# Performance work log

Hardware: AMD Instinct MI355X
Metric: run time of the kernel (lower is better)

The kernel has to match this reference:

```python
import jax, jax.numpy as jnp
import numpy as np

EPS = 1e-8
NUM_HEADS = 8
BELIEF_DIM = 256
TOP_K = 64
DEPTH_BIAS = 0.1


def setup_inputs() -> dict:
    key = jax.random.key(0)
    ks = jax.random.split(key, 12)
    B, T, H = 4, 2048, 2048
    N, D, h = 4096, BELIEF_DIM, NUM_HEADS
    G = 16
    s = 0.02
    return {
        'hidden': jax.random.normal(ks[0], (B, T, H), jnp.float32),
        'active_beliefs': jax.random.normal(ks[1], (N, D), jnp.float32),
        'goal_embeddings': jax.random.normal(ks[2], (G, D), jnp.float32),
        'goal_priorities': jax.random.uniform(ks[3], (G,), jnp.float32),
        'Wq': jax.random.normal(ks[4], (D * h, H), jnp.float32) * s,
        'Wo': jax.random.normal(ks[5], (H, D * h), jnp.float32) * s,
        'Wgoal': jax.random.normal(ks[6], (h, D), jnp.float32) * s,
        'log_temp': jnp.zeros((h,), jnp.float32),
        'Wu': jax.random.normal(ks[7], (H, D * h), jnp.float32) * s,
        'Wg1': jax.random.normal(ks[8], (H // 4, H), jnp.float32) * s,
        'bg1': jnp.zeros((H // 4,), jnp.float32),
        'Wg2': jax.random.normal(ks[9], (1, H // 4), jnp.float32) * s,
        'bg2': jnp.full((1,), 2.0, jnp.float32),  # read_gate_init_bias
        'conv_w': jax.random.normal(ks[10], (D * h, 1, 4), jnp.float32) * s,
    }


def reference(hidden, active_beliefs, goal_embeddings, goal_priorities,
              Wq, Wo, Wgoal, log_temp, Wu, Wg1, bg1, Wg2, bg2, conv_w):
    B, T, H = hidden.shape
    h, D = NUM_HEADS, BELIEF_DIM
    C = h * D

    # hyperspherical decomposition of active beliefs
    radii = jnp.maximum(jnp.linalg.norm(active_beliefs, axis=-1), EPS)  # [N]
    angles = active_beliefs / radii[:, None]                            # [N, D]

    # rough top-k selection (N_active > top_k path)
    mean_q = hidden.mean(axis=(0, 1)) @ Wq.T                 # [h*D]
    rough_q = mean_q.reshape(h, D).mean(axis=0)              # [D]
    rough_scores = angles @ rough_q                          # [N]
    _, topk = jax.lax.top_k(rough_scores, TOP_K)
    keys = angles[topk]              # [K, D]
    values = active_beliefs[topk]    # [K, D]

    # read gate: Linear -> ReLU -> Linear, then signed-sqrt + sigmoid
    g = jax.nn.relu(hidden @ Wg1.T + bg1) @ Wg2.T + bg2      # [B, T, 1]
    g = jnp.sign(g) * jnp.sqrt(jnp.maximum(jnp.abs(g), 1e-6))
    gate = jax.nn.sigmoid(g)

    # per-head queries and temperature-scaled Hopfield scores
    queries = (hidden @ Wq.T).reshape(B, T, h, D)
    temp = jnp.maximum(jnp.exp(log_temp + DEPTH_BIAS), 0.1)  # [h]
    scores = jnp.einsum('bthd,nd->bthn', queries, keys) / jnp.sqrt(jnp.float32(D))
    scores = scores * temp[None, None, :, None]

    # goal-directed bias
    goal_radii = jnp.maximum(jnp.linalg.norm(goal_embeddings, axis=-1), EPS)
    goal_angles = goal_embeddings / goal_radii[:, None]      # [G, D]
    sim = (keys @ goal_angles.T) * goal_priorities[None, :]  # [K, G]
    max_goal_sim = sim.max(axis=-1)                          # [K]
    gate_w = jax.nn.sigmoid(Wgoal @ goal_angles.mean(axis=0))  # [h]
    goal_bias = gate_w[:, None] * max_goal_sim[None, :]      # [h, K]
    scores = scores + goal_bias[None, None, :, :]

    attn = jax.nn.softmax(scores, axis=-1)                   # [B, T, h, K]
    retrieved = jnp.einsum('bthn,nd->bthd', attn, values)    # [B, T, h, D]
    flat = retrieved.reshape(B, T, C)

    # depthwise causal conv (kernel=4, left pad 3) + SiLU fusion
    x = jnp.transpose(flat, (0, 2, 1))                       # [B, C, T]
    conv = jax.lax.conv_general_dilated(
        x, conv_w, window_strides=(1,), padding=[(3, 0)],
        feature_group_count=C, dimension_numbers=('NCH', 'OIH', 'NCH'))
    flat = flat + jax.nn.silu(jnp.transpose(conv, (0, 2, 1)))

    output = gate * (flat @ Wo.T)                            # [B, T, H]
    utility_logits = flat @ Wu.T                             # [B, T, H]
    return output, utility_logits, attn, retrieved
```

## Files before the change

kernel.cpp:

```cpp
#include <hip/hip_runtime.h>


typedef unsigned short ushort_t;
typedef unsigned int   uint_t;

typedef __bf16 bf16x8 __attribute__((ext_vector_type(8)));
typedef float  f32x4  __attribute__((ext_vector_type(4)));
typedef unsigned short u16x8 __attribute__((ext_vector_type(8)));
typedef unsigned short u16x4 __attribute__((ext_vector_type(4)));

#define DI static __device__ __forceinline__

DI ushort_t f2bf(float f) {
    union { float f; uint_t u; } v; v.f = f;
    uint_t u = v.u;
    uint_t r = (u + 0x7FFFu + ((u >> 16) & 1u)) >> 16;
    return (ushort_t)r;
}
DI float bf2f(ushort_t b) {
    union { uint_t u; float f; } v; v.u = ((uint_t)b) << 16;
    return v.f;
}

#define GLL16(gp, lp) __builtin_amdgcn_global_load_lds( \
    (const __attribute__((address_space(1))) void*)(gp), \
    (__attribute__((address_space(3))) void*)(lp), 16, 0, 0)

constexpr int BT  = 8192;
constexpr int Hd  = 2048;
constexpr int Dd  = 256;
constexpr int Cd  = 2048;

constexpr size_t O_HID     = 0;
constexpr size_t O_WQ      = 33554432;
constexpr size_t O_WOWU    = 41943040;
constexpr size_t O_WG1     = 58720256;
constexpr size_t O_QRY     = 60817408;
constexpr size_t O_MEANACC = 94371840;
constexpr size_t O_MEANQ   = 94380032;
constexpr size_t O_RAD     = 94389248;
constexpr size_t O_RSC     = 94405632;
constexpr size_t O_KEYS    = 94422016;
constexpr size_t O_VALT    = 94454784;
constexpr size_t O_GB      = 94487552;
constexpr size_t O_HS      = 94489600;
constexpr size_t O_GP      = 94489856;

__global__ void cast4_kernel(const float* __restrict__ sA, ushort_t* __restrict__ dA, int nA,
                             const float* __restrict__ sB, ushort_t* __restrict__ dB, int nB,
                             const float* __restrict__ sC, ushort_t* __restrict__ dC, int nC,
                             const float* __restrict__ sD, ushort_t* __restrict__ dD, int nD) {
    int total = (nA + nB + nC + nD) >> 2;
    for (int i = blockIdx.x * blockDim.x + threadIdx.x; i < total;
         i += gridDim.x * blockDim.x) {
        int e = i * 4;
        const float* s; ushort_t* d;
        if (e < nA)              { s = sA + e; d = dA + e; }
        else if ((e -= nA) < nB) { s = sB + e; d = dB + e; }
        else if ((e -= nB) < nC) { s = sC + e; d = dC + e; }
        else                     { e -= nC; s = sD + e; d = dD + e; }
        float4 v = *(const float4*)s;
        u16x4 o;
        o[0] = f2bf(v.x); o[1] = f2bf(v.y); o[2] = f2bf(v.z); o[3] = f2bf(v.w);
        *(u16x4*)d = o;
    }
}

__global__ void cast_hidden_kernel(const float* __restrict__ hid, ushort_t* __restrict__ hbf,
                                   float* __restrict__ macc) {
    int r0 = blockIdx.x * 32;
    float s[8];
#pragma unroll
    for (int j = 0; j < 8; ++j) s[j] = 0.f;
    for (int r = 0; r < 32; ++r) {
        const float* rp = hid + (size_t)(r0 + r) * Hd;
        ushort_t*    wp = hbf + (size_t)(r0 + r) * Hd;
#pragma unroll
        for (int j = 0; j < 2; ++j) {
            int c = j * 1024 + threadIdx.x * 4;
            float4 v = *(const float4*)(rp + c);
            s[j*4+0] += v.x; s[j*4+1] += v.y; s[j*4+2] += v.z; s[j*4+3] += v.w;
            u16x4 o;
            o[0] = f2bf(v.x); o[1] = f2bf(v.y); o[2] = f2bf(v.z); o[3] = f2bf(v.w);
            *(u16x4*)(wp + c) = o;
        }
    }
#pragma unroll
    for (int j = 0; j < 2; ++j)
#pragma unroll
        for (int q = 0; q < 4; ++q)
            atomicAdd(macc + j * 1024 + threadIdx.x * 4 + q, s[j*4+q]);
}

__global__ void meanq_kernel(const float* __restrict__ macc, const float* __restrict__ Wq,
                             float* __restrict__ mq) {
    int wid = blockIdx.x * 4 + (threadIdx.x >> 6);
    int lane = threadIdx.x & 63;
    const float inv = 1.f / 8192.f;
    float s = 0.f;
    for (int k = lane; k < Hd; k += 64) s += macc[k] * inv * Wq[(size_t)wid * Hd + k];
#pragma unroll
    for (int m = 32; m; m >>= 1) s += __shfl_xor(s, m, 64);
    if (lane == 0) mq[wid] = s;
}

__global__ void beliefs_kernel(const float* __restrict__ ab, const float* __restrict__ mq,
                               float* __restrict__ radii, float* __restrict__ rsc) {
    int n = blockIdx.x * 4 + (threadIdx.x >> 6);
    int lane = threadIdx.x & 63;
    float rqv[4];
#pragma unroll
    for (int j = 0; j < 4; ++j) {
        int d = lane + 64 * j;
        float s = 0.f;
#pragma unroll
        for (int hh = 0; hh < 8; ++hh) s += mq[hh * 256 + d];
        rqv[j] = s * 0.125f;
    }
    float v[4]; float r2 = 0.f;
#pragma unroll
    for (int j = 0; j < 4; ++j) { v[j] = ab[(size_t)n * Dd + lane + 64 * j]; r2 += v[j] * v[j]; }
#pragma unroll
    for (int m = 32; m; m >>= 1) r2 += __shfl_xor(r2, m, 64);
    float r = fmaxf(sqrtf(r2), 1e-8f);
    float dq = 0.f;
#pragma unroll
    for (int j = 0; j < 4; ++j) dq += (v[j] / r) * rqv[j];
#pragma unroll
    for (int m = 32; m; m >>= 1) dq += __shfl_xor(dq, m, 64);
    if (lane == 0) { radii[n] = r; rsc[n] = dq; }
}

__global__ void topk_kernel(const float* __restrict__ ab, const float* __restrict__ radii,
                            const float* __restrict__ rsc, const float* __restrict__ gemb,
                            const float* __restrict__ gprio, const float* __restrict__ Wgoal,
                            const float* __restrict__ ltemp,
                            ushort_t* __restrict__ keysg, ushort_t* __restrict__ valtg,
                            float* __restrict__ gbias, float* __restrict__ hscale) {
    __shared__ float s_sc[4096];
    __shared__ float s_rv[4];
    __shared__ int   s_ri[4];
    __shared__ int   s_top[64];
    __shared__ float s_ga[16 * 256];
    __shared__ float s_mga[256];
    __shared__ float s_gw[8];
    __shared__ float s_keyf[64 * 256];
    __shared__ float s_red[256];

    int t = threadIdx.x;
    int lane = t & 63, w = t >> 6;
    for (int it = 0; it < 16; ++it) s_sc[t + it * 256] = rsc[t + it * 256];
    __syncthreads();

    for (int kk = 0; kk < 64; ++kk) {
        float bv = -3.4e38f; int bi = 0x7fffffff;
#pragma unroll
        for (int j = 0; j < 16; ++j) {
            int idx = t * 16 + j;
            float v = s_sc[idx];
            if (v > bv || (v == bv && idx < bi)) { bv = v; bi = idx; }
        }
#pragma unroll
        for (int m = 32; m; m >>= 1) {
            float ov = __shfl_xor(bv, m, 64);
            int   oi = __shfl_xor(bi, m, 64);
            if (ov > bv || (ov == bv && oi < bi)) { bv = ov; bi = oi; }
        }
        if (lane == 0) { s_rv[w] = bv; s_ri[w] = bi; }
        __syncthreads();
        if (t == 0) {
            float fv = s_rv[0]; int fi = s_ri[0];
#pragma unroll
            for (int wv = 1; wv < 4; ++wv)
                if (s_rv[wv] > fv || (s_rv[wv] == fv && s_ri[wv] < fi)) { fv = s_rv[wv]; fi = s_ri[wv]; }
            s_top[kk] = fi; s_sc[fi] = -3.4e38f;
        }
        __syncthreads();
    }

    {
        int kk = t >> 2, dp = t & 3;
        int idx = s_top[kk];
        float r = radii[idx];
        for (int dd = 0; dd < 64; ++dd) {
            int d = dp * 64 + dd;
            float v = ab[(size_t)idx * Dd + d];
            float kf = v / r;
            s_keyf[kk * 256 + d] = kf;
            keysg[kk * 256 + d] = f2bf(kf);
            valtg[d * 64 + kk]  = f2bf(v);
        }
    }
    {
        for (int g = w; g < 16; g += 4) {
            float v[4]; float r2 = 0.f;
#pragma unroll
            for (int j = 0; j < 4; ++j) { v[j] = gemb[g * 256 + lane + 64 * j]; r2 += v[j] * v[j]; }
#pragma unroll
            for (int m = 32; m; m >>= 1) r2 += __shfl_xor(r2, m, 64);
            float r = fmaxf(sqrtf(r2), 1e-8f);
#pragma unroll
            for (int j = 0; j < 4; ++j) s_ga[g * 256 + lane + 64 * j] = v[j] / r;
        }
    }
    __syncthreads();
    {
        float s = 0.f;
        for (int g = 0; g < 16; ++g) s += s_ga[g * 256 + t];
        s_mga[t] = s * (1.f / 16.f);
    }
    __syncthreads();
    if (t < 8) {
        float s = 0.f;
        for (int d = 0; d < 256; ++d) s += Wgoal[t * 256 + d] * s_mga[d];
        s_gw[t] = 1.f / (1.f + expf(-s));
        hscale[t] = fmaxf(expf(ltemp[t] + 0.1f), 0.1f) * (1.f / 16.f);
    }
    __syncthreads();
    {
        int kk = t & 63, gq = t >> 6;
        float best = -3.4e38f;
        for (int g = gq * 4; g < gq * 4 + 4; ++g) {
            float dot = 0.f;
            for (int d = 0; d < 256; ++d) dot += s_keyf[kk * 256 + d] * s_ga[g * 256 + d];
            best = fmaxf(best, dot * gprio[g]);
        }
        s_red[t] = best;
    }
    __syncthreads();
    if (t < 64) {
        float m = fmaxf(fmaxf(s_red[t], s_red[t + 64]), fmaxf(s_red[t + 128], s_red[t + 192]));
        for (int hh = 0; hh < 8; ++hh) gbias[hh * 64 + t] = s_gw[hh] * m;
    }
}

template <int EPI>
__global__ __launch_bounds__(256)
void gemm_bt_kernel(const ushort_t* __restrict__ A, const ushort_t* __restrict__ Bw,
                    const ushort_t* __restrict__ Bw2, int Kd,
                    ushort_t* __restrict__ obf, float* __restrict__ of1, float* __restrict__ of2,
                    const float* __restrict__ bg1, const float* __restrict__ Wg2,
                    float* __restrict__ gpart, const float* __restrict__ bg2) {
    __shared__ ushort_t lA[128 * 32];
    __shared__ ushort_t lB[128 * 32];
    const int tid = threadIdx.x;
    const int lane = tid & 63;
    const int w = tid >> 6;
    const int wr = (w >> 1) * 64, wc = (w & 1) * 64;

    const int nwg = gridDim.x * gridDim.y;
    const int lin = blockIdx.y * gridDim.x + blockIdx.x;
    const int swz = (lin & 7) * (nwg >> 3) + (lin >> 3);
    const int bm = (swz / gridDim.x) * 128, bn = (swz % gridDim.x) * 128;

    f32x4 acc[4][4];
#pragma unroll
    for (int mi = 0; mi < 4; ++mi)
#pragma unroll
        for (int ni = 0; ni < 4; ++ni)
#pragma unroll
            for (int q = 0; q < 4; ++q) acc[mi][ni][q] = 0.f;

    const ushort_t* Ab = A + (size_t)bm * Kd;
    const ushort_t* Bb;
    if (EPI == 3 && bn >= 2048) Bb = Bw2 + (size_t)(bn - 2048) * Kd;
    else                        Bb = Bw + (size_t)bn * Kd;
    const int c0 = tid, c1 = tid + 256;

    for (int kt = 0; kt < Kd; kt += 32) {
        __syncthreads();
        GLL16(Ab + (size_t)(c0 >> 2) * Kd + kt + (c0 & 3) * 8, lA + c0 * 8);
        GLL16(Ab + (size_t)(c1 >> 2) * Kd + kt + (c1 & 3) * 8, lA + c1 * 8);
        GLL16(Bb + (size_t)(c0 >> 2) * Kd + kt + (c0 & 3) * 8, lB + c0 * 8);
        GLL16(Bb + (size_t)(c1 >> 2) * Kd + kt + (c1 & 3) * 8, lB + c1 * 8);
        __syncthreads();
        const int ko = (lane >> 4) * 8;
        bf16x8 af[4], bf[4];
#pragma unroll
        for (int mi = 0; mi < 4; ++mi)
            af[mi] = *(const bf16x8*)&lA[(wr + mi * 16 + (lane & 15)) * 32 + ko];
#pragma unroll
        for (int ni = 0; ni < 4; ++ni)
            bf[ni] = *(const bf16x8*)&lB[(wc + ni * 16 + (lane & 15)) * 32 + ko];
#pragma unroll
        for (int mi = 0; mi < 4; ++mi)
#pragma unroll
            for (int ni = 0; ni < 4; ++ni)
                acc[mi][ni] = __builtin_amdgcn_mfma_f32_16x16x32_bf16(af[mi], bf[ni], acc[mi][ni], 0, 0, 0);
    }

    if (EPI == 2) {
        const float b2 = bg2[0];
#pragma unroll
        for (int mi = 0; mi < 4; ++mi)
#pragma unroll
            for (int r = 0; r < 4; ++r) {
                int row = bm + wr + mi * 16 + (lane >> 4) * 4 + r;
                float g = gpart[row] + b2;
                float sg = (g > 0.f) ? 1.f : ((g < 0.f) ? -1.f : 0.f);
                float ss = sg * sqrtf(fmaxf(fabsf(g), 1e-6f));
                float gv = 1.f / (1.f + expf(-ss));
#pragma unroll
                for (int ni = 0; ni < 4; ++ni) {
                    int col = bn + wc + ni * 16 + (lane & 15);
                    float v = acc[mi][ni][r];
                    if (col < 2048) of1[(size_t)row * 2048 + col] = gv * v;
                    else            of2[(size_t)row * 2048 + (col - 2048)] = v;
                }
            }
    } else {
        if (bn < 2048) {
#pragma unroll
            for (int mi = 0; mi < 4; ++mi)
#pragma unroll
                for (int ni = 0; ni < 4; ++ni)
#pragma unroll
                    for (int r = 0; r < 4; ++r) {
                        int row = bm + wr + mi * 16 + (lane >> 4) * 4 + r;
                        int col = bn + wc + ni * 16 + (lane & 15);
                        obf[(size_t)row * 2048 + col] = f2bf(acc[mi][ni][r]);
                    }
        } else {
            float wg[4], bb[4];
#pragma unroll
            for (int ni = 0; ni < 4; ++ni) {
                int col = bn + wc + ni * 16 + (lane & 15) - 2048;
                wg[ni] = Wg2[col]; bb[ni] = bg1[col];
            }
#pragma unroll
            for (int mi = 0; mi < 4; ++mi)
#pragma unroll
                for (int r = 0; r < 4; ++r) {
                    float s = 0.f;
#pragma unroll
                    for (int ni = 0; ni < 4; ++ni) {
                        float v = acc[mi][ni][r] + bb[ni];
                        v = fmaxf(v, 0.f);
                        s += v * wg[ni];
                    }
#pragma unroll
                    for (int m = 8; m; m >>= 1) s += __shfl_xor(s, m, 64);
                    if ((lane & 15) == 0)
                        atomicAdd(gpart + bm + wr + mi * 16 + (lane >> 4) * 4 + r, s);
                }
        }
    }
}

__global__ __launch_bounds__(256, 1)
void attn_kernel(const ushort_t* __restrict__ qry, const ushort_t* __restrict__ keysg,
                 const ushort_t* __restrict__ valtg, const float* __restrict__ gbias,
                 const float* __restrict__ hscale, float* __restrict__ attn_out,
                 float* __restrict__ retr_out, ushort_t* __restrict__ flatb) {
    __shared__ ushort_t sK[64 * 256];
    __shared__ ushort_t sV[256 * 64];
    __shared__ ushort_t sQ[4][32 * 256];
    __shared__ ushort_t sP[4][32 * 64];

    const int tid = threadIdx.x, lane = tid & 63, w = tid >> 6;
    const int r0 = blockIdx.x * 32;

    for (int it = 0; it < 8; ++it) {
        int f = it * 256 + tid;
        int row = f >> 5, cb = f & 31;
        u16x8 v = *(const u16x8*)(keysg + f * 8);
        int byte = (row * 512 + cb * 16) ^ ((row & 7) << 4);
        *(u16x8*)((char*)sK + byte) = v;
    }
    for (int it = 0; it < 8; ++it) {
        int f = it * 256 + tid;
        int row = f >> 3, cb = f & 7;
        u16x8 v = *(const u16x8*)(valtg + f * 8);
        int byte = (row * 128 + cb * 16) ^ ((row & 7) << 4);
        *(u16x8*)((char*)sV + byte) = v;
    }
    __syncthreads();

    char* sQw = (char*)sQ[w];
    char* sPw = (char*)sP[w];

    for (int hi = 0; hi < 2; ++hi) {
        const int head = w * 2 + hi;
        const float hs = hscale[head];
        float gb[4];
#pragma unroll
        for (int ni = 0; ni < 4; ++ni) gb[ni] = gbias[head * 64 + ni * 16 + (lane & 15)];

        for (int it = 0; it < 16; ++it) {
            int f = it * 64 + lane;
            int row = f >> 5, cb = f & 31;
            u16x8 v = *(const u16x8*)(qry + (size_t)(r0 + row) * Cd + head * 256 + cb * 8);
            int byte = (row * 512 + cb * 16) ^ ((row & 7) << 4);
            *(u16x8*)(sQw + byte) = v;
        }

        f32x4 accs[2][4];
#pragma unroll
        for (int mi = 0; mi < 2; ++mi)
#pragma unroll
            for (int ni = 0; ni < 4; ++ni)
#pragma unroll
                for (int q = 0; q < 4; ++q) accs[mi][ni][q] = 0.f;

        for (int kt = 0; kt < 8; ++kt) {
            const int kb = kt * 64 + (lane >> 4) * 16;
            bf16x8 aq[2], bk[4];
#pragma unroll
            for (int mi = 0; mi < 2; ++mi) {
                int m = mi * 16 + (lane & 15);
                aq[mi] = *(const bf16x8*)(sQw + ((m * 512 + kb) ^ ((m & 7) << 4)));
            }
#pragma unroll
            for (int ni = 0; ni < 4; ++ni) {
                int n = ni * 16 + (lane & 15);
                bk[ni] = *(const bf16x8*)((const char*)sK + ((n * 512 + kb) ^ ((n & 7) << 4)));
            }
#pragma unroll
            for (int mi = 0; mi < 2; ++mi)
#pragma unroll
                for (int ni = 0; ni < 4; ++ni)
                    accs[mi][ni] = __builtin_amdgcn_mfma_f32_16x16x32_bf16(aq[mi], bk[ni], accs[mi][ni], 0, 0, 0);
        }

#pragma unroll
        for (int mi = 0; mi < 2; ++mi)
#pragma unroll
            for (int r = 0; r < 4; ++r) {
                float sc[4];
                float mx = -3.4e38f;
#pragma unroll
                for (int ni = 0; ni < 4; ++ni) {
                    sc[ni] = accs[mi][ni][r] * hs + gb[ni];
                    mx = fmaxf(mx, sc[ni]);
                }
#pragma unroll
                for (int m = 8; m; m >>= 1) mx = fmaxf(mx, __shfl_xor(mx, m, 64));
                float p[4]; float sm = 0.f;
#pragma unroll
                for (int ni = 0; ni < 4; ++ni) { p[ni] = expf(sc[ni] - mx); sm += p[ni]; }
#pragma unroll
                for (int m = 8; m; m >>= 1) sm += __shfl_xor(sm, m, 64);
                float inv = 1.f / sm;
                int row = mi * 16 + (lane >> 4) * 4 + r;
                size_t ob = (size_t)(r0 + row) * 512 + head * 64;
#pragma unroll
                for (int ni = 0; ni < 4; ++ni) {
                    float a = p[ni] * inv;
                    int col = ni * 16 + (lane & 15);
                    attn_out[ob + col] = a;
                    int byte = (row * 128 + col * 2) ^ ((row & 7) << 4);
                    *(ushort_t*)(sPw + byte) = f2bf(a);
                }
            }

        f32x4 accr[2][16];
#pragma unroll
        for (int mi = 0; mi < 2; ++mi)
#pragma unroll
            for (int ni = 0; ni < 16; ++ni)
#pragma unroll
                for (int q = 0; q < 4; ++q) accr[mi][ni][q] = 0.f;

#pragma unroll
        for (int kt = 0; kt < 2; ++kt) {
            const int kb = kt * 64 + (lane >> 4) * 16;
            bf16x8 ap[2];
#pragma unroll
            for (int mi = 0; mi < 2; ++mi) {
                int m = mi * 16 + (lane & 15);
                ap[mi] = *(const bf16x8*)(sPw + ((m * 128 + kb) ^ ((m & 7) << 4)));
            }
#pragma unroll
            for (int ni = 0; ni < 16; ++ni) {
                int n = ni * 16 + (lane & 15);
                bf16x8 bv = *(const bf16x8*)((const char*)sV + ((n * 128 + kb) ^ ((n & 7) << 4)));
                accr[0][ni] = __builtin_amdgcn_mfma_f32_16x16x32_bf16(ap[0], bv, accr[0][ni], 0, 0, 0);
                accr[1][ni] = __builtin_amdgcn_mfma_f32_16x16x32_bf16(ap[1], bv, accr[1][ni], 0, 0, 0);
            }
        }

#pragma unroll
        for (int mi = 0; mi < 2; ++mi)
#pragma unroll
            for (int ni = 0; ni < 16; ++ni)
#pragma unroll
                for (int r = 0; r < 4; ++r) {
                    int row = mi * 16 + (lane >> 4) * 4 + r;
                    int d = ni * 16 + (lane & 15);
                    float v = accr[mi][ni][r];
                    size_t o = (size_t)(r0 + row) * Cd + head * 256 + d;
                    retr_out[o] = v;
                    flatb[o] = f2bf(v);
                }
    }
}

__global__ void conv_kernel(const ushort_t* __restrict__ flat, const float* __restrict__ cw,
                            ushort_t* __restrict__ flat2) {
    int cq = blockIdx.x * 256 + threadIdx.x;
    int c  = cq * 4;
    int b  = blockIdx.z;
    int t0 = blockIdx.y * 32;
    float4 wv[4];
#pragma unroll
    for (int j = 0; j < 4; ++j) wv[j] = *(const float4*)(cw + (size_t)(c + j) * 4);
    size_t base = (size_t)b * 2048 * Cd + c;
    float xm3[4], xm2[4], xm1[4];
    if (t0 == 0) {
#pragma unroll
        for (int j = 0; j < 4; ++j) { xm3[j] = 0.f; xm2[j] = 0.f; xm1[j] = 0.f; }
    } else {
        u16x4 a3 = *(const u16x4*)(flat + base + (size_t)(t0 - 3) * Cd);
        u16x4 a2 = *(const u16x4*)(flat + base + (size_t)(t0 - 2) * Cd);
        u16x4 a1 = *(const u16x4*)(flat + base + (size_t)(t0 - 1) * Cd);
#pragma unroll
        for (int j = 0; j < 4; ++j) { xm3[j] = bf2f(a3[j]); xm2[j] = bf2f(a2[j]); xm1[j] = bf2f(a1[j]); }
    }
    for (int t = t0; t < t0 + 32; ++t) {
        u16x4 xv = *(const u16x4*)(flat + base + (size_t)t * Cd);
        u16x4 ov;
#pragma unroll
        for (int j = 0; j < 4; ++j) {
            float x = bf2f(xv[j]);
            float cv = wv[j].x * xm3[j] + wv[j].y * xm2[j] + wv[j].z * xm1[j] + wv[j].w * x;
            float sl = cv / (1.f + expf(-cv));
            ov[j] = f2bf(x + sl);
            xm3[j] = xm2[j]; xm2[j] = xm1[j]; xm1[j] = x;
        }
        *(u16x4*)(flat2 + base + (size_t)t * Cd) = ov;
    }
}

extern "C" void kernel_launch(void* const* d_in, const int* in_sizes, int n_in,
                              void* d_out, int out_size, void* d_ws, size_t ws_size,
                              hipStream_t stream) {
    (void)in_sizes; (void)n_in; (void)out_size; (void)ws_size;
    const float* hid   = (const float*)d_in[0];
    const float* ab    = (const float*)d_in[1];
    const float* gemb  = (const float*)d_in[2];
    const float* gprio = (const float*)d_in[3];
    const float* Wq    = (const float*)d_in[4];
    const float* Wo    = (const float*)d_in[5];
    const float* Wgoal = (const float*)d_in[6];
    const float* ltemp = (const float*)d_in[7];
    const float* Wu    = (const float*)d_in[8];
    const float* Wg1   = (const float*)d_in[9];
    const float* bg1   = (const float*)d_in[10];
    const float* Wg2   = (const float*)d_in[11];
    const float* bg2   = (const float*)d_in[12];
    const float* cw    = (const float*)d_in[13];

    float* out      = (float*)d_out;
    float* out_util = out + 16777216;
    float* out_attn = out + 33554432;
    float* out_retr = out + 37748736;

    char* ws = (char*)d_ws;
    ushort_t* hbf    = (ushort_t*)(ws + O_HID);
    ushort_t* wqb    = (ushort_t*)(ws + O_WQ);
    ushort_t* wowub  = (ushort_t*)(ws + O_WOWU);
    ushort_t* wg1b   = (ushort_t*)(ws + O_WG1);
    ushort_t* qryb   = (ushort_t*)(ws + O_QRY);
    ushort_t* flatb  = hbf;
    float* macc   = (float*)(ws + O_MEANACC);
    float* meanq  = (float*)(ws + O_MEANQ);
    float* radii  = (float*)(ws + O_RAD);
    float* rsc    = (float*)(ws + O_RSC);
    ushort_t* keysb = (ushort_t*)(ws + O_KEYS);
    ushort_t* valtb = (ushort_t*)(ws + O_VALT);
    float* gbias  = (float*)(ws + O_GB);
    float* hscale = (float*)(ws + O_HS);
    float* gpart  = (float*)(ws + O_GP);

    hipMemsetAsync(ws + O_MEANACC, 0, 2048 * 4, stream);
    hipMemsetAsync(ws + O_GP, 0, 8192 * 4, stream);

    cast_hidden_kernel<<<256, 256, 0, stream>>>(hid, hbf, macc);
    cast4_kernel<<<2048, 256, 0, stream>>>(Wq, wqb, 2048 * 2048,
                                           Wo, wowub, 2048 * 2048,
                                           Wu, wowub + 2048 * 2048, 2048 * 2048,
                                           Wg1, wg1b, 512 * 2048);

    meanq_kernel<<<512, 256, 0, stream>>>(macc, Wq, meanq);
    beliefs_kernel<<<1024, 256, 0, stream>>>(ab, meanq, radii, rsc);
    topk_kernel<<<1, 256, 0, stream>>>(ab, radii, rsc, gemb, gprio, Wgoal, ltemp,
                                       keysb, valtb, gbias, hscale);

    gemm_bt_kernel<3><<<dim3(20, 64), 256, 0, stream>>>(hbf, wqb, wg1b, 2048,
        qryb, nullptr, nullptr, bg1, Wg2, gpart, nullptr);

    attn_kernel<<<256, 256, 0, stream>>>(qryb, keysb, valtb, gbias, hscale,
                                         out_attn, out_retr, flatb);

    conv_kernel<<<dim3(2, 64, 4), 256, 0, stream>>>(flatb, cw, qryb );

    gemm_bt_kernel<2><<<dim3(32, 64), 256, 0, stream>>>(qryb, wowub, nullptr, 2048,
        nullptr, out, out_util, nullptr, nullptr, gpart, bg2);
}
```

Before: 894.5 us.

## Split attention heads across grid, drop Q staging, vectorize topk and cast

```diff
diff --git a/kernel.cpp b/kernel.cpp
--- a/kernel.cpp
+++ b/kernel.cpp
@@ -68,11 +68,11 @@
 
 __global__ void cast_hidden_kernel(const float* __restrict__ hid, ushort_t* __restrict__ hbf,
                                    float* __restrict__ macc) {
-    int r0 = blockIdx.x * 32;
+    int r0 = blockIdx.x * 16;
     float s[8];
 #pragma unroll
     for (int j = 0; j < 8; ++j) s[j] = 0.f;
-    for (int r = 0; r < 32; ++r) {
+    for (int r = 0; r < 16; ++r) {
         const float* rp = hid + (size_t)(r0 + r) * Hd;
         ushort_t*    wp = hbf + (size_t)(r0 + r) * Hd;
 #pragma unroll
@@ -155,10 +155,14 @@
     for (int kk = 0; kk < 64; ++kk) {
         float bv = -3.4e38f; int bi = 0x7fffffff;
 #pragma unroll
-        for (int j = 0; j < 16; ++j) {
-            int idx = t * 16 + j;
-            float v = s_sc[idx];
-            if (v > bv || (v == bv && idx < bi)) { bv = v; bi = idx; }
+        for (int j4 = 0; j4 < 4; ++j4) {
+            f32x4 v4 = *(const f32x4*)&s_sc[t * 16 + j4 * 4];
+#pragma unroll
+            for (int q = 0; q < 4; ++q) {
+                int idx = t * 16 + j4 * 4 + q;
+                float v = v4[q];
+                if (v > bv || (v == bv && idx < bi)) { bv = v; bi = idx; }
+            }
         }
 #pragma unroll
         for (int m = 32; m; m >>= 1) {
@@ -182,13 +186,23 @@
         int kk = t >> 2, dp = t & 3;
         int idx = s_top[kk];
         float r = radii[idx];
-        for (int dd = 0; dd < 64; ++dd) {
-            int d = dp * 64 + dd;
-            float v = ab[(size_t)idx * Dd + d];
-            float kf = v / r;
-            s_keyf[kk * 256 + d] = kf;
-            keysg[kk * 256 + d] = f2bf(kf);
-            valtg[d * 64 + kk]  = f2bf(v);
+        const float4* src = (const float4*)(ab + (size_t)idx * Dd + dp * 64);
+#pragma unroll 4
+        for (int dd = 0; dd < 16; ++dd) {
+            float4 v = src[dd];
+            int d = dp * 64 + dd * 4;
+            float k0 = v.x / r, k1 = v.y / r, k2 = v.z / r, k3 = v.w / r;
+            s_keyf[kk * 256 + d + 0] = k0;
+            s_keyf[kk * 256 + d + 1] = k1;
+            s_keyf[kk * 256 + d + 2] = k2;
+            s_keyf[kk * 256 + d + 3] = k3;
+            u16x4 o;
+            o[0] = f2bf(k0); o[1] = f2bf(k1); o[2] = f2bf(k2); o[3] = f2bf(k3);
+            *(u16x4*)(keysg + kk * 256 + d) = o;
+            valtg[(d + 0) * 64 + kk] = f2bf(v.x);
+            valtg[(d + 1) * 64 + kk] = f2bf(v.y);
+            valtg[(d + 2) * 64 + kk] = f2bf(v.z);
+            valtg[(d + 3) * 64 + kk] = f2bf(v.w);
         }
     }
     {
@@ -219,10 +233,15 @@
     __syncthreads();
     {
         int kk = t & 63, gq = t >> 6;
+        const f32x4* kp = (const f32x4*)&s_keyf[kk * 256];
         float best = -3.4e38f;
         for (int g = gq * 4; g < gq * 4 + 4; ++g) {
+            const f32x4* gp_ = (const f32x4*)&s_ga[g * 256];
             float dot = 0.f;
-            for (int d = 0; d < 256; ++d) dot += s_keyf[kk * 256 + d] * s_ga[g * 256 + d];
+            for (int d4 = 0; d4 < 64; ++d4) {
+                f32x4 a = kp[d4], b = gp_[d4];
+                dot += a[0] * b[0] + a[1] * b[1] + a[2] * b[2] + a[3] * b[3];
+            }
             best = fmaxf(best, dot * gprio[g]);
         }
         s_red[t] = best;
@@ -347,18 +366,18 @@
     }
 }
 
-__global__ __launch_bounds__(256, 1)
+__global__ __launch_bounds__(256, 2)
 void attn_kernel(const ushort_t* __restrict__ qry, const ushort_t* __restrict__ keysg,
                  const ushort_t* __restrict__ valtg, const float* __restrict__ gbias,
                  const float* __restrict__ hscale, float* __restrict__ attn_out,
                  float* __restrict__ retr_out, ushort_t* __restrict__ flatb) {
     __shared__ ushort_t sK[64 * 256];
     __shared__ ushort_t sV[256 * 64];
-    __shared__ ushort_t sQ[4][32 * 256];
     __shared__ ushort_t sP[4][32 * 64];
 
     const int tid = threadIdx.x, lane = tid & 63, w = tid >> 6;
     const int r0 = blockIdx.x * 32;
+    const int head = blockIdx.y * 4 + w;
 
     for (int it = 0; it < 8; ++it) {
         int f = it * 256 + tid;
@@ -376,123 +395,112 @@
     }
     __syncthreads();
 
-    char* sQw = (char*)sQ[w];
     char* sPw = (char*)sP[w];
-
-    for (int hi = 0; hi < 2; ++hi) {
-        const int head = w * 2 + hi;
-        const float hs = hscale[head];
-        float gb[4];
-#pragma unroll
-        for (int ni = 0; ni < 4; ++ni) gb[ni] = gbias[head * 64 + ni * 16 + (lane & 15)];
-
-        for (int it = 0; it < 16; ++it) {
-            int f = it * 64 + lane;
-            int row = f >> 5, cb = f & 31;
-            u16x8 v = *(const u16x8*)(qry + (size_t)(r0 + row) * Cd + head * 256 + cb * 8);
-            int byte = (row * 512 + cb * 16) ^ ((row & 7) << 4);
-            *(u16x8*)(sQw + byte) = v;
-        }
-
-        f32x4 accs[2][4];
+    const float hs = hscale[head];
+    float gb[4];
+#pragma unroll
+    for (int ni = 0; ni < 4; ++ni) gb[ni] = gbias[head * 64 + ni * 16 + (lane & 15)];
+
+    const ushort_t* qbase = qry + (size_t)r0 * Cd + head * 256
+                          + (size_t)(lane & 15) * Cd + (lane >> 4) * 8;
+
+    f32x4 accs[2][4];
+#pragma unroll
+    for (int mi = 0; mi < 2; ++mi)
+#pragma unroll
+        for (int ni = 0; ni < 4; ++ni)
+#pragma unroll
+            for (int q = 0; q < 4; ++q) accs[mi][ni][q] = 0.f;
+
+#pragma unroll
+    for (int kt = 0; kt < 8; ++kt) {
+        const int kb = kt * 64 + (lane >> 4) * 16;
+        bf16x8 aq[2], bk[4];
 #pragma unroll
         for (int mi = 0; mi < 2; ++mi)
+            aq[mi] = *(const bf16x8*)(qbase + (size_t)(mi * 16) * Cd + kt * 32);
+#pragma unroll
+        for (int ni = 0; ni < 4; ++ni) {
+            int n = ni * 16 + (lane & 15);
+            bk[ni] = *(const bf16x8*)((const char*)sK + ((n * 512 + kb) ^ ((n & 7) << 4)));
+        }
+#pragma unroll
+        for (int mi = 0; mi < 2; ++mi)
 #pragma unroll
             for (int ni = 0; ni < 4; ++ni)
-#pragma unroll
-                for (int q = 0; q < 4; ++q) accs[mi][ni][q] = 0.f;
-
-        for (int kt = 0; kt < 8; ++kt) {
-            const int kb = kt * 64 + (lane >> 4) * 16;
-            bf16x8 aq[2], bk[4];
-#pragma unroll
-            for (int mi = 0; mi < 2; ++mi) {
-                int m = mi * 16 + (lane & 15);
-                aq[mi] = *(const bf16x8*)(sQw + ((m * 512 + kb) ^ ((m & 7) << 4)));
+                accs[mi][ni] = __builtin_amdgcn_mfma_f32_16x16x32_bf16(aq[mi], bk[ni], accs[mi][ni], 0, 0, 0);
+    }
+
+#pragma unroll
+    for (int mi = 0; mi < 2; ++mi)
+#pragma unroll
+        for (int r = 0; r < 4; ++r) {
+            float sc[4];
+            float mx = -3.4e38f;
+#pragma unroll
+            for (int ni = 0; ni < 4; ++ni) {
+                sc[ni] = accs[mi][ni][r] * hs + gb[ni];
+                mx = fmaxf(mx, sc[ni]);
             }
 #pragma unroll
+            for (int m = 8; m; m >>= 1) mx = fmaxf(mx, __shfl_xor(mx, m, 64));
+            float p[4]; float sm = 0.f;
+#pragma unroll
+            for (int ni = 0; ni < 4; ++ni) { p[ni] = expf(sc[ni] - mx); sm += p[ni]; }
+#pragma unroll
+            for (int m = 8; m; m >>= 1) sm += __shfl_xor(sm, m, 64);
+            float inv = 1.f / sm;
+            int row = mi * 16 + (lane >> 4) * 4 + r;
+            size_t ob = (size_t)(r0 + row) * 512 + head * 64;
+#pragma unroll
             for (int ni = 0; ni < 4; ++ni) {
-                int n = ni * 16 + (lane & 15);
-                bk[ni] = *(const bf16x8*)((const char*)sK + ((n * 512 + kb) ^ ((n & 7) << 4)));
+                float a = p[ni] * inv;
+                int col = ni * 16 + (lane & 15);
+                attn_out[ob + col] = a;
+                int byte = (row * 128 + col * 2) ^ ((row & 7) << 4);
+                *(ushort_t*)(sPw + byte) = f2bf(a);
             }
-#pragma unroll
-            for (int mi = 0; mi < 2; ++mi)
-#pragma unroll
-                for (int ni = 0; ni < 4; ++ni)
-                    accs[mi][ni] = __builtin_amdgcn_mfma_f32_16x16x32_bf16(aq[mi], bk[ni], accs[mi][ni], 0, 0, 0);
-        }
-
-#pragma unroll
-        for (int mi = 0; mi < 2; ++mi)
+        }
+
+    f32x4 accr[2][16];
+#pragma unroll
+    for (int mi = 0; mi < 2; ++mi)
+#pragma unroll
+        for (int ni = 0; ni < 16; ++ni)
+#pragma unroll
+            for (int q = 0; q < 4; ++q) accr[mi][ni][q] = 0.f;
+
+#pragma unroll
+    for (int kt = 0; kt < 2; ++kt) {
+        const int kb = kt * 64 + (lane >> 4) * 16;
+        bf16x8 ap[2];
+#pragma unroll
+        for (int mi = 0; mi < 2; ++mi) {
+            int m = mi * 16 + (lane & 15);
+            ap[mi] = *(const bf16x8*)(sPw + ((m * 128 + kb) ^ ((m & 7) << 4)));
+        }
+#pragma unroll
+        for (int ni = 0; ni < 16; ++ni) {
+            int n = ni * 16 + (lane & 15);
+            bf16x8 bv = *(const bf16x8*)((const char*)sV + ((n * 128 + kb) ^ ((n & 7) << 4)));
+            accr[0][ni] = __builtin_amdgcn_mfma_f32_16x16x32_bf16(ap[0], bv, accr[0][ni], 0, 0, 0);
+            accr[1][ni] = __builtin_amdgcn_mfma_f32_16x16x32_bf16(ap[1], bv, accr[1][ni], 0, 0, 0);
+        }
+    }
+
+#pragma unroll
+    for (int mi = 0; mi < 2; ++mi)
+#pragma unroll
+        for (int ni = 0; ni < 16; ++ni)
 #pragma unroll
             for (int r = 0; r < 4; ++r) {
-                float sc[4];
-                float mx = -3.4e38f;
-#pragma unroll
-                for (int ni = 0; ni < 4; ++ni) {
-                    sc[ni] = accs[mi][ni][r] * hs + gb[ni];
-                    mx = fmaxf(mx, sc[ni]);
-                }
-#pragma unroll
-                for (int m = 8; m; m >>= 1) mx = fmaxf(mx, __shfl_xor(mx, m, 64));
-                float p[4]; float sm = 0.f;
-#pragma unroll
-                for (int ni = 0; ni < 4; ++ni) { p[ni] = expf(sc[ni] - mx); sm += p[ni]; }
-#pragma unroll
-                for (int m = 8; m; m >>= 1) sm += __shfl_xor(sm, m, 64);
-                float inv = 1.f / sm;
                 int row = mi * 16 + (lane >> 4) * 4 + r;
-                size_t ob = (size_t)(r0 + row) * 512 + head * 64;
-#pragma unroll
-                for (int ni = 0; ni < 4; ++ni) {
-                    float a = p[ni] * inv;
-                    int col = ni * 16 + (lane & 15);
-                    attn_out[ob + col] = a;
-                    int byte = (row * 128 + col * 2) ^ ((row & 7) << 4);
-                    *(ushort_t*)(sPw + byte) = f2bf(a);
-                }
+                int d = ni * 16 + (lane & 15);
+                float v = accr[mi][ni][r];
+                size_t o = (size_t)(r0 + row) * Cd + head * 256 + d;
+                retr_out[o] = v;
+                flatb[o] = f2bf(v);
             }
-
-        f32x4 accr[2][16];
-#pragma unroll
-        for (int mi = 0; mi < 2; ++mi)
-#pragma unroll
-            for (int ni = 0; ni < 16; ++ni)
-#pragma unroll
-                for (int q = 0; q < 4; ++q) accr[mi][ni][q] = 0.f;
-
-#pragma unroll
-        for (int kt = 0; kt < 2; ++kt) {
-            const int kb = kt * 64 + (lane >> 4) * 16;
-            bf16x8 ap[2];
-#pragma unroll
-            for (int mi = 0; mi < 2; ++mi) {
-                int m = mi * 16 + (lane & 15);
-                ap[mi] = *(const bf16x8*)(sPw + ((m * 128 + kb) ^ ((m & 7) << 4)));
-            }
-#pragma unroll
-            for (int ni = 0; ni < 16; ++ni) {
-                int n = ni * 16 + (lane & 15);
-                bf16x8 bv = *(const bf16x8*)((const char*)sV + ((n * 128 + kb) ^ ((n & 7) << 4)));
-                accr[0][ni] = __builtin_amdgcn_mfma_f32_16x16x32_bf16(ap[0], bv, accr[0][ni], 0, 0, 0);
-                accr[1][ni] = __builtin_amdgcn_mfma_f32_16x16x32_bf16(ap[1], bv, accr[1][ni], 0, 0, 0);
-            }
-        }
-
-#pragma unroll
-        for (int mi = 0; mi < 2; ++mi)
-#pragma unroll
-            for (int ni = 0; ni < 16; ++ni)
-#pragma unroll
-                for (int r = 0; r < 4; ++r) {
-                    int row = mi * 16 + (lane >> 4) * 4 + r;
-                    int d = ni * 16 + (lane & 15);
-                    float v = accr[mi][ni][r];
-                    size_t o = (size_t)(r0 + row) * Cd + head * 256 + d;
-                    retr_out[o] = v;
-                    flatb[o] = f2bf(v);
-                }
-    }
 }
 
 __global__ void conv_kernel(const ushort_t* __restrict__ flat, const float* __restrict__ cw,
@@ -575,7 +583,7 @@
     hipMemsetAsync(ws + O_MEANACC, 0, 2048 * 4, stream);
     hipMemsetAsync(ws + O_GP, 0, 8192 * 4, stream);
 
-    cast_hidden_kernel<<<256, 256, 0, stream>>>(hid, hbf, macc);
+    cast_hidden_kernel<<<512, 256, 0, stream>>>(hid, hbf, macc);
     cast4_kernel<<<2048, 256, 0, stream>>>(Wq, wqb, 2048 * 2048,
                                            Wo, wowub, 2048 * 2048,
                                            Wu, wowub + 2048 * 2048, 2048 * 2048,
@@ -589,8 +597,8 @@
     gemm_bt_kernel<3><<<dim3(20, 64), 256, 0, stream>>>(hbf, wqb, wg1b, 2048,
         qryb, nullptr, nullptr, bg1, Wg2, gpart, nullptr);
 
-    attn_kernel<<<256, 256, 0, stream>>>(qryb, keysb, valtb, gbias, hscale,
-                                         out_attn, out_retr, flatb);
+    attn_kernel<<<dim3(256, 2), 256, 0, stream>>>(qryb, keysb, valtb, gbias, hscale,
+                                                  out_attn, out_retr, flatb);
 
     conv_kernel<<<dim3(2, 64, 4), 256, 0, stream>>>(flatb, cw, qryb );
 
```

New measurement: 904.3 us. No clear change (+1.1%).
